# Kernel optimization log

Hardware: AMD Instinct MI355X
Metric: run time of the kernel (lower is better)

The kernel has to match this reference:

```python
import jax, jax.numpy as jnp
import numpy as np

B, N, D_IN, D_OUT = 4, 2048, 1024, 1024


def setup_inputs() -> dict:
    key = jax.random.key(0)
    kx, kq, kk, kv = jax.random.split(key, 4)
    x = jax.random.normal(kx, (B, N, D_IN), dtype=jnp.float32)
    # torch Linear(d_in, d_out, bias=False): y = x @ W.T, W ~ U(-1/sqrt(d_in), 1/sqrt(d_in)).
    # Store as [d_in, d_out] so y = x @ W.
    bound = 1.0 / np.sqrt(D_IN)
    Wq = jax.random.uniform(kq, (D_IN, D_OUT), jnp.float32, -bound, bound)
    Wk = jax.random.uniform(kk, (D_IN, D_OUT), jnp.float32, -bound, bound)
    Wv = jax.random.uniform(kv, (D_IN, D_OUT), jnp.float32, -bound, bound)
    return {"x": x, "Wq": Wq, "Wk": Wk, "Wv": Wv}


def reference(x, Wq, Wk, Wv):
    # x: [B, N, d_in]
    q = jnp.einsum("bnd,de->bne", x, Wq)  # [B, N, d_out]
    k = jnp.einsum("bnd,de->bne", x, Wk)
    v = jnp.einsum("bnd,de->bne", x, Wv)
    n = x.shape[1]
    scores = jnp.einsum("bqe,bke->bqk", q, k)  # [B, N, N]
    causal = jnp.triu(jnp.ones((n, n), dtype=bool), k=1)  # True above diagonal -> masked
    scores = jnp.where(causal, -jnp.inf, scores)
    scale = 1.0 / jnp.sqrt(jnp.asarray(k.shape[-1], dtype=scores.dtype))
    weights = jax.nn.softmax(scores * scale, axis=-1)
    # dropout with drop_rate=0.0 is identity
    return jnp.einsum("bqk,bke->bqe", weights, v)  # [B, N, d_out]
```

## Files before the change

### kernel.cpp

```cpp
#include <hip/hip_runtime.h>

typedef float  f4v  __attribute__((ext_vector_type(4)));
typedef short  s8v  __attribute__((ext_vector_type(8)));

__device__ __forceinline__ ushort f2b(float f) {
    union { float f; unsigned int u; } v; v.f = f;
    unsigned int u = v.u;
    u += 0x7fffu + ((u >> 16) & 1u);
    return (ushort)(u >> 16);
}
__device__ __forceinline__ float b2f(ushort u) {
    union { unsigned int u; float f; } v; v.u = ((unsigned int)u) << 16;
    return v.f;
}

__device__ __forceinline__ void async16(const ushort* g, ushort* ldsp) {
    __builtin_amdgcn_global_load_lds(
        (const __attribute__((address_space(1))) unsigned int*)g,
        (__attribute__((address_space(3))) unsigned int*)ldsp, 16, 0, 0);
}

__global__ __launch_bounds__(256) void cast_f32_bf16(const float* __restrict__ in,
                                                     ushort* __restrict__ out,
                                                     float* __restrict__ l, int n4) {
    int i = blockIdx.x * 256 + threadIdx.x;
    if (i < 8192) l[i] = 0.f;
    if (i < n4) {
        float4 f = ((const float4*)in)[i];
        ushort4 o;
        o.x = f2b(f.x); o.y = f2b(f.y); o.z = f2b(f.z); o.w = f2b(f.w);
        ((ushort4*)out)[i] = o;
    }
}

__global__ __launch_bounds__(256) void transpose_cast(const float* __restrict__ w0,
                                                      const float* __restrict__ w1,
                                                      const float* __restrict__ w2,
                                                      ushort* __restrict__ out) {
    __shared__ float tile[32][33];
    const float* W = (blockIdx.z == 0) ? w0 : (blockIdx.z == 1 ? w1 : w2);
    ushort* O = out + (size_t)blockIdx.z * (1024u * 1024u);
    int x0 = blockIdx.x * 32, y0 = blockIdx.y * 32;
    int tx = threadIdx.x, ty = threadIdx.y;
    for (int i = 0; i < 4; i++)
        tile[ty + i * 8][tx] = W[(size_t)(y0 + ty + i * 8) * 1024 + x0 + tx];
    __syncthreads();
    for (int i = 0; i < 4; i++)
        O[(size_t)(x0 + ty + i * 8) * 1024 + y0 + tx] = f2b(tile[tx][ty + i * 8]);
}

#define GEMM_KLOOP64(ArowP_, BrowP_, strideA_, strideB_, K0_, KMAX_)                  \
    for (int k0 = (K0_); k0 < (KMAX_); k0 += 64) {                                    \
        async16(ArowP_ + k0, sAw);                                                    \
        async16(ArowP_ + k0 + 16 * (strideA_), sAw + 16 * 32);                        \
        async16(ArowP_ + k0 + 32, sAw + 4096);                                        \
        async16(ArowP_ + k0 + 32 + 16 * (strideA_), sAw + 4096 + 16 * 32);            \
        async16(BrowP_ + k0, sBw);                                                    \
        async16(BrowP_ + k0 + 16 * (strideB_), sBw + 16 * 32);                        \
        async16(BrowP_ + k0 + 32, sBw + 4096);                                        \
        async16(BrowP_ + k0 + 32 + 16 * (strideB_), sBw + 4096 + 16 * 32);            \
        __syncthreads();                                                              \
        for (int s = 0; s < 2; s++) {                                                 \
            s8v af[4], bf[4];                                                         \
            for (int mi = 0; mi < 4; mi++)                                            \
                af[mi] = *(const s8v*)&sA[s * 4096 + (wm + mi * 16 + l16) * 32 + quad * 8]; \
            for (int ni = 0; ni < 4; ni++)                                            \
                bf[ni] = *(const s8v*)&sB[s * 4096 + (wn + ni * 16 + l16) * 32 + quad * 8]; \
            for (int mi = 0; mi < 4; mi++)                                            \
                for (int ni = 0; ni < 4; ni++)                                        \
                    acc[mi][ni] = __builtin_amdgcn_mfma_f32_16x16x32_bf16(            \
                        af[mi], bf[ni], acc[mi][ni], 0, 0, 0);                        \
        }                                                                             \
        __syncthreads();                                                              \
    }

#define GEMM_KLOOP64_N64(ArowP_, BrowP_, strideA_, strideB_, K0_, KMAX_)              \
    for (int k0 = (K0_); k0 < (KMAX_); k0 += 64) {                                    \
        async16(ArowP_ + k0, sAw);                                                    \
        async16(ArowP_ + k0 + 16 * (strideA_), sAw + 16 * 32);                        \
        async16(ArowP_ + k0 + 32, sAw + 4096);                                        \
        async16(ArowP_ + k0 + 32 + 16 * (strideA_), sAw + 4096 + 16 * 32);            \
        async16(BrowP_ + k0, sBw);                                                    \
        async16(BrowP_ + k0 + 32, sBw + 2048);                                        \
        __syncthreads();                                                              \
        for (int s = 0; s < 2; s++) {                                                 \
            s8v af[4], bf[2];                                                         \
            for (int mi = 0; mi < 4; mi++)                                            \
                af[mi] = *(const s8v*)&sA[s * 4096 + (wm + mi * 16 + l16) * 32 + quad * 8]; \
            for (int ni = 0; ni < 2; ni++)                                            \
                bf[ni] = *(const s8v*)&sB[s * 2048 + (wn + ni * 16 + l16) * 32 + quad * 8]; \
            for (int mi = 0; mi < 4; mi++)                                            \
                for (int ni = 0; ni < 2; ni++)                                        \
                    acc[mi][ni] = __builtin_amdgcn_mfma_f32_16x16x32_bf16(            \
                        af[mi], bf[ni], acc[mi][ni], 0, 0, 0);                        \
        }                                                                             \
        __syncthreads();                                                              \
    }

#define GEMM_PREAMBLE                                                                 \
    const int tid = threadIdx.x;                                                      \
    const int w = tid >> 6, lane = tid & 63, quad = lane >> 4, l16 = lane & 15;       \
    const int wm = (w >> 1) * 64, wn = (w & 1) * 64;                                  \
    f4v acc[4][4];                                                                    \
    for (int mi = 0; mi < 4; mi++)                                                    \
        for (int ni = 0; ni < 4; ni++) acc[mi][ni] = 0;                               \
    ushort* sAw = &sA[(w * 32) * 32];                                                 \
    ushort* sBw = &sB[(w * 32) * 32];

#define GEMM_PREAMBLE_N64                                                             \
    const int tid = threadIdx.x;                                                      \
    const int w = tid >> 6, lane = tid & 63, quad = lane >> 4, l16 = lane & 15;       \
    const int wm = (w >> 1) * 64, wn = (w & 1) * 32;                                  \
    f4v acc[4][2];                                                                    \
    for (int mi = 0; mi < 4; mi++)                                                    \
        for (int ni = 0; ni < 2; ni++) acc[mi][ni] = 0;                               \
    ushort* sAw = &sA[(w * 32) * 32];                                                 \
    ushort* sBw = &sB[(w * 16) * 32];

__global__ __launch_bounds__(256) void gemm_qkv(const ushort* __restrict__ A,
                                                const ushort* __restrict__ Wt,
                                                ushort* __restrict__ q,
                                                ushort* __restrict__ k,
                                                ushort* __restrict__ vt) {
    constexpr int K = 1024;
    __shared__ ushort sA[2 * 4096];
    __shared__ ushort sB[2 * 4096];
    const int L = blockIdx.x;
    const int t = (L & 7) * 192 + (L >> 3);
    const int z = t >> 9;
    const int r = t & 511;
    const int g = r >> 5, h = r & 31;
    const int m0 = (g * 4 + (h >> 3)) * 128;
    const int n0 = (h & 7) * 128;
    const ushort* Bt = Wt + (size_t)z * 1024 * 1024;
    GEMM_PREAMBLE
    const ushort* ArowP = A + (size_t)(m0 + w * 32 + (lane >> 2)) * K + (lane & 3) * 8;
    const ushort* BrowP = Bt + (size_t)(n0 + w * 32 + (lane >> 2)) * K + (lane & 3) * 8;
    GEMM_KLOOP64(ArowP, BrowP, K, K, 0, K)

    if (z < 2) {
        ushort* C = (z == 0) ? q : k;
        for (int mi = 0; mi < 4; mi++)
            for (int ni = 0; ni < 4; ni++) {
                int row = m0 + wm + mi * 16 + quad * 4;
                int col = n0 + wn + ni * 16 + l16;
                f4v v = acc[mi][ni];
                for (int rr = 0; rr < 4; rr++)
                    C[(size_t)(row + rr) * 1024 + col] = f2b(v[rr]);
            }
    } else {
        for (int mi = 0; mi < 4; mi++)
            for (int ni = 0; ni < 4; ni++) {
                int row = m0 + wm + mi * 16 + quad * 4;
                int col = n0 + wn + ni * 16 + l16;
                f4v v = acc[mi][ni];
                int b = row >> 11, tok = row & 2047;
                ushort4 pk;
                pk.x = f2b(v[0]); pk.y = f2b(v[1]); pk.z = f2b(v[2]); pk.w = f2b(v[3]);
                *(ushort4*)&vt[(size_t)b * (1024u * 2048u) + (size_t)col * 2048 + tok] = pk;
            }
    }
}

__global__ __launch_bounds__(256) void sgemm_qk(const ushort* __restrict__ Q,
                                                const ushort* __restrict__ Km,
                                                ushort* __restrict__ E,
                                                float* __restrict__ l) {
    constexpr int K = 1024;
    __shared__ ushort sA[2 * 4096];
    __shared__ ushort sB[2 * 2048];
    const int L = blockIdx.x;
    const int t = (L & 7) * 136 + (L >> 3);
    const int b = t / 272;
    const int tt = t - b * 272;
    int mt = 0;
    while ((mt + 1) * (mt + 2) <= tt) mt++;
    const int nt = tt - mt * (mt + 1);
    const ushort* A  = Q  + (size_t)b * 2048 * 1024;
    const ushort* Bt = Km + (size_t)b * 2048 * 1024;
    ushort* C = E + (size_t)b * 2048 * 2048;
    float* lb = l + (size_t)b * 2048;
    const int m0 = mt * 128, n0 = nt * 64;
    GEMM_PREAMBLE_N64
    const ushort* ArowP = A + (size_t)(m0 + w * 32 + (lane >> 2)) * K + (lane & 3) * 8;
    const ushort* BrowP = Bt + (size_t)(n0 + w * 16 + (lane >> 2)) * K + (lane & 3) * 8;
    GEMM_KLOOP64_N64(ArowP, BrowP, K, K, 0, K)

    for (int mi = 0; mi < 4; mi++) {
        for (int rr = 0; rr < 4; rr++) {
            const int row = m0 + wm + mi * 16 + quad * 4 + rr;
            float s = 0.f;
            for (int ni = 0; ni < 2; ni++) {
                int col = n0 + wn + ni * 16 + l16;
                float e = (col <= row) ? __expf(acc[mi][ni][rr] * 0.03125f) : 0.f;
                ushort eb = f2b(e);
                C[(size_t)row * 2048 + col] = eb;
                s += b2f(eb);
            }
            s += __shfl_xor(s, 1);
            s += __shfl_xor(s, 2);
            s += __shfl_xor(s, 4);
            s += __shfl_xor(s, 8);
            if (l16 == 0) atomicAdd(&lb[row], s);
        }
    }
}

__global__ __launch_bounds__(256) void gemm_pv(const ushort* __restrict__ Em,
                                               const ushort* __restrict__ Vt,
                                               const float* __restrict__ l,
                                               float* __restrict__ Out) {
    __shared__ ushort sA[2 * 4096];
    __shared__ ushort sB[2 * 2048];
    const int L = blockIdx.x;
    const int t = (L & 7) * 128 + (L >> 3);
    const int b = t >> 8;
    const int r = t & 255;
    const int qq = r >> 4;
    const int nt = r & 15;
    const int mt = (qq & 1) ? (qq >> 1) : (15 - (qq >> 1));
    const ushort* A  = Em + (size_t)b * 2048 * 2048;
    const ushort* Bt = Vt + (size_t)b * 1024 * 2048;
    const float* lb = l + (size_t)b * 2048;
    float* C = Out + (size_t)b * 2048 * 1024;
    const int m0 = mt * 128, n0 = nt * 64;
    const int Kmax = m0 + 128;
    GEMM_PREAMBLE_N64
    const ushort* ArowP = A + (size_t)(m0 + w * 32 + (lane >> 2)) * 2048 + (lane & 3) * 8;
    const ushort* BrowP = Bt + (size_t)(n0 + w * 16 + (lane >> 2)) * 2048 + (lane & 3) * 8;
    GEMM_KLOOP64_N64(ArowP, BrowP, 2048, 2048, 0, Kmax)

    for (int mi = 0; mi < 4; mi++) {
        const int row = m0 + wm + mi * 16 + quad * 4;
        float inv[4];
        for (int rr = 0; rr < 4; rr++) inv[rr] = 1.f / lb[row + rr];
        for (int ni = 0; ni < 2; ni++) {
            int col = n0 + wn + ni * 16 + l16;
            f4v v = acc[mi][ni];
            for (int rr = 0; rr < 4; rr++)
                C[(size_t)(row + rr) * 1024 + col] = v[rr] * inv[rr];
        }
    }
}

extern "C" void kernel_launch(void* const* d_in, const int* in_sizes, int n_in,
                              void* d_out, int out_size, void* d_ws, size_t ws_size,
                              hipStream_t stream) {
    const float* x  = (const float*)d_in[0];
    const float* Wq = (const float*)d_in[1];
    const float* Wk = (const float*)d_in[2];
    const float* Wv = (const float*)d_in[3];
    float* out = (float*)d_out;

    char* ws = (char*)d_ws;
    const size_t MiB = 1u << 20;
    ushort* xb = (ushort*)(ws);
    ushort* wt = (ushort*)(ws + 16 * MiB);
    ushort* q  = (ushort*)(ws + 22 * MiB);
    ushort* k  = (ushort*)(ws + 38 * MiB);
    ushort* vt = (ushort*)(ws + 54 * MiB);
    ushort* E  = (ushort*)(ws + 70 * MiB);
    float*  l  = (float*)(ws + 102 * MiB);

    cast_f32_bf16<<<(8192 * 1024 / 4) / 256, 256, 0, stream>>>(x, xb, l, 8192 * 1024 / 4);
    transpose_cast<<<dim3(32, 32, 3), dim3(32, 8), 0, stream>>>(Wq, Wk, Wv, wt);

    gemm_qkv<<<1536, 256, 0, stream>>>(xb, wt, q, k, vt);
    sgemm_qk<<<1088, 256, 0, stream>>>(q, k, E, l);
    gemm_pv<<<1024, 256, 0, stream>>>(E, vt, l, out);
}
```

Before: 230.2 us.

## Rewrite QKV GEMM with 256x128 tiles, triple-buffered LDS and swizzle

The QKV projection GEMM moves from 128x128 tiles with 256 threads and a single-stage load/sync loop to 256x128 tiles with 512 threads. It uses a three-stage async global-to-LDS pipeline in 147 KB of dynamic shared memory, an XOR-swizzled LDS layout, split MFMA phases with raised wave priority, and an XCD-aware tile mapping. The aim is to hide global load latency behind MFMA work, avoid LDS bank conflicts, and raise data reuse per tile. In exchange it needs large LDS, which limits occupancy, and hand-written waitcnt/barrier scheduling that could be fragile.

```diff
diff --git a/kernel.cpp b/kernel.cpp
--- a/kernel.cpp
+++ b/kernel.cpp
@@ -48,31 +48,6 @@
     for (int i = 0; i < 4; i++)
         O[(size_t)(x0 + ty + i * 8) * 1024 + y0 + tx] = f2b(tile[tx][ty + i * 8]);
 }
-
-#define GEMM_KLOOP64(ArowP_, BrowP_, strideA_, strideB_, K0_, KMAX_)                  \
-    for (int k0 = (K0_); k0 < (KMAX_); k0 += 64) {                                    \
-        async16(ArowP_ + k0, sAw);                                                    \
-        async16(ArowP_ + k0 + 16 * (strideA_), sAw + 16 * 32);                        \
-        async16(ArowP_ + k0 + 32, sAw + 4096);                                        \
-        async16(ArowP_ + k0 + 32 + 16 * (strideA_), sAw + 4096 + 16 * 32);            \
-        async16(BrowP_ + k0, sBw);                                                    \
-        async16(BrowP_ + k0 + 16 * (strideB_), sBw + 16 * 32);                        \
-        async16(BrowP_ + k0 + 32, sBw + 4096);                                        \
-        async16(BrowP_ + k0 + 32 + 16 * (strideB_), sBw + 4096 + 16 * 32);            \
-        __syncthreads();                                                              \
-        for (int s = 0; s < 2; s++) {                                                 \
-            s8v af[4], bf[4];                                                         \
-            for (int mi = 0; mi < 4; mi++)                                            \
-                af[mi] = *(const s8v*)&sA[s * 4096 + (wm + mi * 16 + l16) * 32 + quad * 8]; \
-            for (int ni = 0; ni < 4; ni++)                                            \
-                bf[ni] = *(const s8v*)&sB[s * 4096 + (wn + ni * 16 + l16) * 32 + quad * 8]; \
-            for (int mi = 0; mi < 4; mi++)                                            \
-                for (int ni = 0; ni < 4; ni++)                                        \
-                    acc[mi][ni] = __builtin_amdgcn_mfma_f32_16x16x32_bf16(            \
-                        af[mi], bf[ni], acc[mi][ni], 0, 0, 0);                        \
-        }                                                                             \
-        __syncthreads();                                                              \
-    }
 
 #define GEMM_KLOOP64_N64(ArowP_, BrowP_, strideA_, strideB_, K0_, KMAX_)              \
     for (int k0 = (K0_); k0 < (KMAX_); k0 += 64) {                                    \
@@ -97,16 +72,6 @@
         __syncthreads();                                                              \
     }
 
-#define GEMM_PREAMBLE                                                                 \
-    const int tid = threadIdx.x;                                                      \
-    const int w = tid >> 6, lane = tid & 63, quad = lane >> 4, l16 = lane & 15;       \
-    const int wm = (w >> 1) * 64, wn = (w & 1) * 64;                                  \
-    f4v acc[4][4];                                                                    \
-    for (int mi = 0; mi < 4; mi++)                                                    \
-        for (int ni = 0; ni < 4; ni++) acc[mi][ni] = 0;                               \
-    ushort* sAw = &sA[(w * 32) * 32];                                                 \
-    ushort* sBw = &sB[(w * 32) * 32];
-
 #define GEMM_PREAMBLE_N64                                                             \
     const int tid = threadIdx.x;                                                      \
     const int w = tid >> 6, lane = tid & 63, quad = lane >> 4, l16 = lane & 15;       \
@@ -117,39 +82,138 @@
     ushort* sAw = &sA[(w * 32) * 32];                                                 \
     ushort* sBw = &sB[(w * 16) * 32];
 
-__global__ __launch_bounds__(256) void gemm_qkv(const ushort* __restrict__ A,
-                                                const ushort* __restrict__ Wt,
-                                                ushort* __restrict__ q,
-                                                ushort* __restrict__ k,
-                                                ushort* __restrict__ vt) {
+__global__ __launch_bounds__(512, 2) void gemm_qkv(const ushort* __restrict__ A,
+                                                   const ushort* __restrict__ Wt,
+                                                   ushort* __restrict__ q,
+                                                   ushort* __restrict__ k,
+                                                   ushort* __restrict__ vt) {
     constexpr int K = 1024;
-    __shared__ ushort sA[2 * 4096];
-    __shared__ ushort sB[2 * 4096];
+    extern __shared__ ushort lds[];
+
     const int L = blockIdx.x;
-    const int t = (L & 7) * 192 + (L >> 3);
-    const int z = t >> 9;
-    const int r = t & 511;
-    const int g = r >> 5, h = r & 31;
-    const int m0 = (g * 4 + (h >> 3)) * 128;
-    const int n0 = (h & 7) * 128;
+    const int xcd = L & 7, idx = L >> 3;
+    const int ci = xcd >> 1, cj = xcd & 1;
+    const int mo = idx / 12, no = idx - mo * 12;
+    const int mt = ci * 8 + mo;
+    const int ntile = cj * 12 + no;
+    const int z = ntile >> 3;
+    const int m0 = mt * 256;
+    const int n0 = (ntile & 7) * 128;
     const ushort* Bt = Wt + (size_t)z * 1024 * 1024;
-    GEMM_PREAMBLE
-    const ushort* ArowP = A + (size_t)(m0 + w * 32 + (lane >> 2)) * K + (lane & 3) * 8;
-    const ushort* BrowP = Bt + (size_t)(n0 + w * 32 + (lane >> 2)) * K + (lane & 3) * 8;
-    GEMM_KLOOP64(ArowP, BrowP, K, K, 0, K)
+
+    const int tid = threadIdx.x;
+    const int w = tid >> 6, lane = tid & 63, quad = lane >> 4, l16 = lane & 15;
+    const int wm = (w >> 1) * 64, wn = (w & 1) * 64;
+
+    ushort* a0 = lds;           ushort* b0 = lds + 16384;
+    ushort* a1 = lds + 24576;   ushort* b1 = lds + 40960;
+    ushort* a2 = lds + 49152;   ushort* b2 = lds + 65536;
+
+    const int lr = lane >> 3;
+    const int lc8 = (lane & 7) ^ lr;
+    const ushort* Ab = A  + (size_t)(m0 + w * 8 + lr) * K + lc8 * 8;
+    const ushort* Bb = Bt + (size_t)(n0 + w * 8 + lr) * K + lc8 * 8;
+    const int dW = w * 512;
+
+    f4v acc[4][4];
+    #pragma unroll
+    for (int mi = 0; mi < 4; mi++)
+        #pragma unroll
+        for (int ni = 0; ni < 4; ni++) acc[mi][ni] = 0;
+
+    #pragma unroll
+    for (int a = 0; a < 4; a++) async16(Ab + (size_t)a * 64 * K,      a0 + a * 4096 + dW);
+    #pragma unroll
+    for (int b = 0; b < 2; b++) async16(Bb + (size_t)b * 64 * K,      b0 + b * 4096 + dW);
+    #pragma unroll
+    for (int a = 0; a < 4; a++) async16(Ab + (size_t)a * 64 * K + 64, a1 + a * 4096 + dW);
+    #pragma unroll
+    for (int b = 0; b < 2; b++) async16(Bb + (size_t)b * 64 * K + 64, b1 + b * 4096 + dW);
+    asm volatile("s_waitcnt vmcnt(6)" ::: "memory");
+    asm volatile("s_barrier" ::: "memory");
+
+    for (int t = 0; t < 16; ++t) {
+        const int k2 = (t + 2) * 64;
+        s8v af[4][2], bf[2][2];
+
+        #pragma unroll
+        for (int mi = 0; mi < 4; mi++)
+            #pragma unroll
+            for (int s = 0; s < 2; s++)
+                af[mi][s] = *(const s8v*)&a0[(wm + mi * 16 + l16) * 64 +
+                                             (((s * 4 + quad) ^ (l16 & 7)) * 8)];
+        #pragma unroll
+        for (int ni = 0; ni < 2; ni++)
+            #pragma unroll
+            for (int s = 0; s < 2; s++)
+                bf[ni][s] = *(const s8v*)&b0[(wn + ni * 16 + l16) * 64 +
+                                             (((s * 4 + quad) ^ (l16 & 7)) * 8)];
+        if (t < 14) {
+            async16(Ab + (size_t)0 * 64 * K + k2, a2 + 0 * 4096 + dW);
+            async16(Ab + (size_t)1 * 64 * K + k2, a2 + 1 * 4096 + dW);
+            async16(Ab + (size_t)2 * 64 * K + k2, a2 + 2 * 4096 + dW);
+        }
+        asm volatile("s_barrier" ::: "memory");
+        __builtin_amdgcn_s_setprio(1);
+        #pragma unroll
+        for (int mi = 0; mi < 4; mi++)
+            #pragma unroll
+            for (int ni = 0; ni < 2; ni++)
+                #pragma unroll
+                for (int s = 0; s < 2; s++)
+                    acc[mi][ni] = __builtin_amdgcn_mfma_f32_16x16x32_bf16(
+                        af[mi][s], bf[ni][s], acc[mi][ni], 0, 0, 0);
+        __builtin_amdgcn_s_setprio(0);
+        asm volatile("s_barrier" ::: "memory");
+
+        #pragma unroll
+        for (int ni = 0; ni < 2; ni++)
+            #pragma unroll
+            for (int s = 0; s < 2; s++)
+                bf[ni][s] = *(const s8v*)&b0[(wn + (ni + 2) * 16 + l16) * 64 +
+                                             (((s * 4 + quad) ^ (l16 & 7)) * 8)];
+        if (t < 14) {
+            async16(Ab + (size_t)3 * 64 * K + k2, a2 + 3 * 4096 + dW);
+            async16(Bb + (size_t)0 * 64 * K + k2, b2 + 0 * 4096 + dW);
+            async16(Bb + (size_t)1 * 64 * K + k2, b2 + 1 * 4096 + dW);
+        }
+        asm volatile("s_barrier" ::: "memory");
+        __builtin_amdgcn_s_setprio(1);
+        #pragma unroll
+        for (int mi = 0; mi < 4; mi++)
+            #pragma unroll
+            for (int ni = 0; ni < 2; ni++)
+                #pragma unroll
+                for (int s = 0; s < 2; s++)
+                    acc[mi][ni + 2] = __builtin_amdgcn_mfma_f32_16x16x32_bf16(
+                        af[mi][s], bf[ni][s], acc[mi][ni + 2], 0, 0, 0);
+        __builtin_amdgcn_s_setprio(0);
+
+        if (t < 14)       asm volatile("s_waitcnt vmcnt(6)" ::: "memory");
+        else if (t == 14) asm volatile("s_waitcnt vmcnt(0)" ::: "memory");
+        asm volatile("s_barrier" ::: "memory");
+
+        ushort* ta = a0; a0 = a1; a1 = a2; a2 = ta;
+        ushort* tb = b0; b0 = b1; b1 = b2; b2 = tb;
+    }
 
     if (z < 2) {
         ushort* C = (z == 0) ? q : k;
-        for (int mi = 0; mi < 4; mi++)
+        #pragma unroll
+        for (int mi = 0; mi < 4; mi++)
+            #pragma unroll
             for (int ni = 0; ni < 4; ni++) {
                 int row = m0 + wm + mi * 16 + quad * 4;
                 int col = n0 + wn + ni * 16 + l16;
                 f4v v = acc[mi][ni];
+                #pragma unroll
                 for (int rr = 0; rr < 4; rr++)
                     C[(size_t)(row + rr) * 1024 + col] = f2b(v[rr]);
             }
     } else {
-        for (int mi = 0; mi < 4; mi++)
+        #pragma unroll
+        for (int mi = 0; mi < 4; mi++)
+            #pragma unroll
             for (int ni = 0; ni < 4; ni++) {
                 int row = m0 + wm + mi * 16 + quad * 4;
                 int col = n0 + wn + ni * 16 + l16;
@@ -252,6 +316,13 @@
     const float* Wv = (const float*)d_in[3];
     float* out = (float*)d_out;
 
+    static bool init = false;
+    if (!init) {
+        hipFuncSetAttribute(reinterpret_cast<const void*>(gemm_qkv),
+                            hipFuncAttributeMaxDynamicSharedMemorySize, 147456);
+        init = true;
+    }
+
     char* ws = (char*)d_ws;
     const size_t MiB = 1u << 20;
     ushort* xb = (ushort*)(ws);
@@ -265,7 +336,7 @@
     cast_f32_bf16<<<(8192 * 1024 / 4) / 256, 256, 0, stream>>>(x, xb, l, 8192 * 1024 / 4);
     transpose_cast<<<dim3(32, 32, 3), dim3(32, 8), 0, stream>>>(Wq, Wk, Wv, wt);
 
-    gemm_qkv<<<1536, 256, 0, stream>>>(xb, wt, q, k, vt);
+    gemm_qkv<<<768, 512, 147456, stream>>>(xb, wt, q, k, vt);
     sgemm_qk<<<1088, 256, 0, stream>>>(q, k, E, l);
     gemm_pv<<<1024, 256, 0, stream>>>(E, vt, l, out);
 }
```

Result: no change. 232.1 us (+0.8%).
